# Kernel tuning notes

Hardware: AMD Instinct MI355X
Metric: run time of the kernel (lower is better)

The kernel has to match this reference:

```python
import jax, jax.numpy as jnp
import numpy as np
from jax import lax

B, N, S, K = 16, 8192, 1024, 32
FACTOR = 1.0
EPS_BN = 1e-5


def farthest_point_sample(xyz, npoint):
    # xyz: [B, N, 3] -> idx [B, npoint]. Deterministic start at index 0
    # (torch version starts at a random index; start choice doesn't change the math pattern).
    b, n, _ = xyz.shape
    bidx = jnp.arange(b)

    def step(carry, _):
        distance, farthest = carry
        centroid = xyz[bidx, farthest]                      # [B, 3]
        dist = jnp.sum((xyz - centroid[:, None, :]) ** 2, -1)  # [B, N]
        distance = jnp.minimum(distance, dist)
        new_far = jnp.argmax(distance, axis=-1)
        return (distance, new_far), farthest

    init = (jnp.full((b, n), 1e10, xyz.dtype), jnp.zeros((b,), jnp.int32))
    _, idxs = lax.scan(step, init, None, length=npoint)
    return idxs.T  # [B, npoint]


def square_distance(src, dst):
    # [B,Ns,3] x [B,Nd,3] -> [B,Ns,Nd]
    d = -2.0 * jnp.einsum('bnc,bmc->bnm', src, dst)
    d += jnp.sum(src ** 2, -1)[:, :, None]
    d += jnp.sum(dst ** 2, -1)[:, None, :]
    return d


def safe_cdist(x):
    # x: [B, C, S]; pairwise euclidean over rows -> [B, C, C]; zero-safe sqrt
    diff = x[:, :, None, :] - x[:, None, :, :]          # [B, C, C, S]
    sq = jnp.sum(diff * diff, -1)
    pos = sq > 0
    return jnp.where(pos, jnp.sqrt(jnp.where(pos, sq, 1.0)), 0.0)


def batchnorm(x, gamma, beta, axes):
    mean = jnp.mean(x, axes, keepdims=True)
    var = jnp.var(x, axes, keepdims=True)  # biased, as in torch BN normalization
    return (x - mean) / jnp.sqrt(var + EPS_BN) * gamma + beta


def reference(xyz, bn1_gamma, bn1_beta, bn2_gamma, bn2_beta):
    b = xyz.shape[0]
    # --- FPS sampling ---
    fps_idx = farthest_point_sample(lax.stop_gradient(xyz), S)          # [B,S]
    new_xyz = jnp.take_along_axis(xyz, fps_idx[:, :, None], axis=1)     # [B,S,3]
    # --- kNN grouping ---
    sq = square_distance(lax.stop_gradient(new_xyz), lax.stop_gradient(xyz))  # [B,S,N]
    _, knn_idx = lax.top_k(-sq, K)                                      # [B,S,K] indices
    grouped = jax.vmap(lambda p, i: p[i])(xyz, knn_idx)                 # [B,S,K,3]
    diff = grouped - new_xyz[:, :, None, :]
    std = jnp.std(diff, ddof=1)                                         # scalar, unbiased like torch.std
    knn_norm = diff / (std + 1e-5)
    center = jnp.broadcast_to(new_xyz[:, :, None, :], (b, S, K, 3))
    knn_xyz = jnp.concatenate([knn_norm, center], axis=-1)              # [B,S,K,6]
    # --- Pooling over neighbors ---
    x = jnp.transpose(knn_xyz, (0, 3, 1, 2))                            # [B,6,S,K]
    lc = jnp.max(x, -1) + jnp.mean(x, -1)                               # [B,6,S]
    lc = jax.nn.relu(batchnorm(lc, bn1_gamma[None, :, None], bn1_beta[None, :, None], (0, 2)))
    # --- Consecutive representation (cdist + superdiagonal factor) ---
    tfcw = safe_cdist(lc)                                               # [B,6,6]
    i = jnp.arange(5)
    tfcw = tfcw.at[:, i, i + 1].multiply(FACTOR)
    # --- Pooling2 ---
    feat = tfcw.reshape(b, -1)                                          # [B,36]
    feat = jax.nn.relu(batchnorm(feat, bn2_gamma[None, :], bn2_beta[None, :], (0,)))
    return feat


def setup_inputs() -> dict:
    key = jax.random.key(0)
    k1, = jax.random.split(key, 1)
    return {
        'xyz': jax.random.normal(k1, (B, N, 3), dtype=jnp.float32),
        'bn1_gamma': jnp.ones((6,), jnp.float32),
        'bn1_beta': jnp.zeros((6,), jnp.float32),
        'bn2_gamma': jnp.ones((36,), jnp.float32),
        'bn2_beta': jnp.zeros((36,), jnp.float32),
    }
```

## Files before the change

kernel.cpp:

```cpp
#include <hip/hip_runtime.h>
#include <hip/hip_bf16.h>

constexpr int BB = 16;
constexpr int NN = 8192;
constexpr int SS = 1024;
constexpr int KK = 32;
constexpr int BUFC = 256;

__device__ __forceinline__ float b2f(__hip_bfloat16 h) { return __bfloat162float(h); }

__device__ __forceinline__ unsigned mkey32(float d) {
    unsigned u = __float_as_uint(d);
    return u ^ (0x80000000u | (unsigned)((int)u >> 31));
}

template <int CTRL, int RMASK>
__device__ __forceinline__ unsigned long long dppmove_u64(unsigned long long v) {
    int lo = (int)(unsigned)v, hi = (int)(unsigned)(v >> 32);
    int nlo = __builtin_amdgcn_update_dpp(lo, lo, CTRL, RMASK, 0xf, false);
    int nhi = __builtin_amdgcn_update_dpp(hi, hi, CTRL, RMASK, 0xf, false);
    return ((unsigned long long)(unsigned)nhi << 32) | (unsigned)nlo;
}

__device__ __forceinline__ unsigned long long u64max(unsigned long long a,
                                                     unsigned long long b) {
    return a > b ? a : b;
}

__device__ __forceinline__ unsigned long long wave_max_dpp(unsigned long long k) {
    k = u64max(k, dppmove_u64<0x121, 0xf>(k));
    k = u64max(k, dppmove_u64<0x122, 0xf>(k));
    k = u64max(k, dppmove_u64<0x124, 0xf>(k));
    k = u64max(k, dppmove_u64<0x128, 0xf>(k));
    k = u64max(k, dppmove_u64<0x142, 0xa>(k));
    k = u64max(k, dppmove_u64<0x143, 0xc>(k));
    return k;
}

__device__ __forceinline__ unsigned long long bitonic64(unsigned long long v, int lane) {
#pragma unroll
    for (int k = 2; k <= 64; k <<= 1) {
#pragma unroll
        for (int j = k >> 1; j > 0; j >>= 1) {
            unsigned long long p = __shfl_xor(v, j);
            bool up = ((lane & k) == 0);
            bool lower = ((lane & j) == 0);
            bool take_min = (up == lower);
            v = take_min ? (p < v ? p : v) : (p > v ? p : v);
        }
    }
    return v;
}

__global__ __launch_bounds__(256) void convert_kernel(
    const void* __restrict__ xyz_raw, const void* __restrict__ g1r,
    const void* __restrict__ b1r, const void* __restrict__ g2r,
    const void* __restrict__ b2r, float* __restrict__ xyzf,
    float* __restrict__ params, void* __restrict__ out_raw) {
    const unsigned short* u = (const unsigned short*)xyz_raw;
    unsigned short s = u[2 * (threadIdx.x & 63)];
    int e = (s >> 7) & 0xFF;
    unsigned long long m = __ballot(e >= 100 && e <= 140);
    bool isbf = __popcll(m) > 48;

    const int NT = BB * NN * 3;
    int tid = blockIdx.x * blockDim.x + threadIdx.x;
    int stride = gridDim.x * blockDim.x;
    if (isbf) {
        const __hip_bfloat16* p = (const __hip_bfloat16*)xyz_raw;
        for (int i = tid; i < NT; i += stride) xyzf[i] = b2f(p[i]);
    } else {
        const float* p = (const float*)xyz_raw;
        for (int i = tid; i < NT; i += stride) xyzf[i] = p[i];
    }
    if (blockIdx.x == 0 && threadIdx.x < 85) {
        int t = threadIdx.x;
        if (t == 84) {
            params[84] = isbf ? 1.0f : 0.0f;
        } else {
            const void* src; int off;
            if (t < 6)       { src = g1r; off = t; }
            else if (t < 12) { src = b1r; off = t - 6; }
            else if (t < 48) { src = g2r; off = t - 12; }
            else             { src = b2r; off = t - 48; }
            params[t] = isbf ? b2f(((const __hip_bfloat16*)src)[off])
                             : ((const float*)src)[off];
        }
    }
    if (blockIdx.x == 1 && threadIdx.x < 64) {
        for (int i = threadIdx.x; i < 576; i += 64) {
            if (isbf) ((__hip_bfloat16*)out_raw)[i] = __float2bfloat16(1.0f);
            else      ((float*)out_raw)[i] = 1.0f;
        }
    }
}

__global__ __launch_bounds__(512, 2) void fps_kernel(const float* __restrict__ xyzf,
                                                     float* __restrict__ new_xyz) {
    constexpr int T = 512, P = NN / T;
    const int b = blockIdx.x, t = threadIdx.x;
    const float* xb = xyzf + (size_t)b * NN * 3;

    float px[P], py[P], pz[P], ds[P];
#pragma unroll
    for (int j = 0; j < P; j++) {
        int p = t + j * T;
        px[j] = xb[p * 3 + 0];
        py[j] = xb[p * 3 + 1];
        pz[j] = xb[p * 3 + 2];
        ds[j] = 1e10f;
    }

    __shared__ unsigned long long skey[2][8];

    float cx = xb[0], cy = xb[1], cz = xb[2];
    if (t == 0) {
        float* o = new_xyz + (size_t)b * SS * 3;
        o[0] = cx; o[1] = cy; o[2] = cz;
    }
    const int wave = t >> 6, lane = t & 63;

    for (int step = 1; step < SS; step++) {
        float bv = -1.0f; int bj = 0;
#pragma unroll
        for (int j = 0; j < P; j++) {
            float dx = __fsub_rn(px[j], cx);
            float dy = __fsub_rn(py[j], cy);
            float dz = __fsub_rn(pz[j], cz);
            float d = __fadd_rn(__fadd_rn(__fmul_rn(dx, dx), __fmul_rn(dy, dy)), __fmul_rn(dz, dz));
            float mm = fminf(ds[j], d);
            ds[j] = mm;
            if (mm > bv) { bv = mm; bj = j; }
        }
        unsigned idx = (unsigned)(t + bj * T);
        unsigned long long key =
            ((unsigned long long)__float_as_uint(bv) << 32) | (unsigned)(~idx);

        key = wave_max_dpp(key);
        const int par = step & 1;
        if (lane == 63) skey[par][wave] = key;
        __syncthreads();

        unsigned long long k0 = u64max(skey[par][0], skey[par][1]);
        unsigned long long k1 = u64max(skey[par][2], skey[par][3]);
        unsigned long long k2 = u64max(skey[par][4], skey[par][5]);
        unsigned long long k3 = u64max(skey[par][6], skey[par][7]);
        unsigned long long bk = u64max(u64max(k0, k1), u64max(k2, k3));

        unsigned gidx = ~(unsigned)bk;
        const float* cp = xb + (size_t)gidx * 3;
        cx = cp[0]; cy = cp[1]; cz = cp[2];
        if (t == 0) {
            float* o = new_xyz + ((size_t)b * SS + step) * 3;
            o[0] = cx; o[1] = cy; o[2] = cz;
        }
    }
}

__global__ __launch_bounds__(256, 2) void knn_kernel(const float* __restrict__ xyzf,
                                                     const float* __restrict__ new_xyz,
                                                     float* __restrict__ A,
                                                     double* __restrict__ qstats) {
    __shared__ unsigned long long buf[4][BUFC];
    const int t = threadIdx.x;
    const int lane = t & 63, wv = t >> 6;
    const int w = blockIdx.x * 4 + wv;
    const int b = w >> 10, s = w & 1023;

    const float* q = new_xyz + ((size_t)b * SS + s) * 3;
    float qx = q[0], qy = q[1], qz = q[2];
    float qq = __fadd_rn(__fadd_rn(__fmul_rn(qx, qx), __fmul_rn(qy, qy)), __fmul_rn(qz, qz));

    const float* pb = xyzf + (size_t)b * NN * 3;

    unsigned mk[128];
    unsigned long long lmin = ~0ull;
#pragma unroll
    for (int j = 0; j < 128; j++) {
        int idx = j * 64 + lane;
        float px = pb[idx * 3 + 0];
        float py = pb[idx * 3 + 1];
        float pz = pb[idx * 3 + 2];
        float dot = __fadd_rn(__fadd_rn(__fmul_rn(qx, px), __fmul_rn(qy, py)), __fmul_rn(qz, pz));
        float pp  = __fadd_rn(__fadd_rn(__fmul_rn(px, px), __fmul_rn(py, py)), __fmul_rn(pz, pz));
        float d = __fadd_rn(__fadd_rn(__fmul_rn(-2.0f, dot), qq), pp);
        mk[j] = mkey32(d);
        unsigned long long key = ((unsigned long long)mk[j] << 32) | (unsigned)idx;
        lmin = key < lmin ? key : lmin;
    }

    unsigned long long vs = bitonic64(lmin, lane);
    unsigned long long That = __shfl(vs, 31);

    for (int i = lane; i < BUFC; i += 64) buf[wv][i] = ~0ull;
    const unsigned long long ltmask = (1ull << lane) - 1ull;
    int base = 0;
#pragma unroll
    for (int j = 0; j < 128; j++) {
        unsigned long long key = ((unsigned long long)mk[j] << 32) | (unsigned)(j * 64 + lane);
        bool f = key <= That;
        unsigned long long bal = __ballot(f);
        int pos = base + __popcll(bal & ltmask);
        if (f && pos < BUFC) buf[wv][pos] = key;
        base += __popcll(bal);
    }

    if (base > BUFC) {
        unsigned lo = 0, hi = (unsigned)(That >> 32);
        for (int it = 0; it < 32; it++) {
            unsigned mid = lo + ((hi - lo) >> 1);
            int c = 0;
#pragma unroll
            for (int j = 0; j < 128; j++) c += (mk[j] <= mid) ? 1 : 0;
#pragma unroll
            for (int o = 32; o > 0; o >>= 1) c += __shfl_xor(c, o);
            if (c >= 32) hi = mid; else lo = mid + 1;
        }
        That = ((unsigned long long)hi << 32) | 0xFFFFFFFFull;
        for (int i = lane; i < BUFC; i += 64) buf[wv][i] = ~0ull;
        base = 0;
#pragma unroll
        for (int j = 0; j < 128; j++) {
            unsigned long long key = ((unsigned long long)mk[j] << 32) | (unsigned)(j * 64 + lane);
            bool f = key <= That;
            unsigned long long bal = __ballot(f);
            int pos = base + __popcll(bal & ltmask);
            if (f && pos < BUFC) buf[wv][pos] = key;
            base += __popcll(bal);
        }
        if (base > BUFC) base = BUFC;
    }

    int M = base;
    unsigned long long kept = ~0ull;
    if (M <= 64) {
        unsigned long long v = (lane < M) ? buf[wv][lane] : ~0ull;
        v = bitonic64(v, lane);
        kept = v;
    } else {
        unsigned long long c0 = buf[wv][lane];
        unsigned long long c1 = buf[wv][64 + lane];
        unsigned long long c2 = buf[wv][128 + lane];
        unsigned long long c3 = buf[wv][192 + lane];
        for (int r = 0; r < KK; r++) {
            unsigned long long m01 = c0 < c1 ? c0 : c1;
            unsigned long long m23 = c2 < c3 ? c2 : c3;
            unsigned long long mm = m01 < m23 ? m01 : m23;
#pragma unroll
            for (int o = 32; o > 0; o >>= 1) {
                unsigned long long t2 = __shfl_xor(mm, o);
                mm = t2 < mm ? t2 : mm;
            }
            if (lane == r) kept = mm;
            c0 = (c0 == mm) ? ~0ull : c0;
            c1 = (c1 == mm) ? ~0ull : c1;
            c2 = (c2 == mm) ? ~0ull : c2;
            c3 = (c3 == mm) ? ~0ull : c3;
        }
    }

    bool act = (lane < KK);
    float gx = 0.0f, gy = 0.0f, gz = 0.0f;
    if (act) {
        unsigned nidx = (unsigned)kept;
        gx = pb[nidx * 3 + 0];
        gy = pb[nidx * 3 + 1];
        gz = pb[nidx * 3 + 2];
    }
    float dx = __fsub_rn(gx, qx);
    float dy = __fsub_rn(gy, qy);
    float dz = __fsub_rn(gz, qz);
    float mx = act ? dx : -3.402823466e38f;
    float my = act ? dy : -3.402823466e38f;
    float mz = act ? dz : -3.402823466e38f;
    float sx = act ? dx : 0.0f;
    float sy = act ? dy : 0.0f;
    float sz = act ? dz : 0.0f;
    double s1 = act ? ((double)dx + (double)dy + (double)dz) : 0.0;
    double s2 = act ? ((double)dx * dx + (double)dy * dy + (double)dz * dz) : 0.0;
#pragma unroll
    for (int o = 32; o > 0; o >>= 1) {
        mx = fmaxf(mx, __shfl_xor(mx, o));
        my = fmaxf(my, __shfl_xor(my, o));
        mz = fmaxf(mz, __shfl_xor(mz, o));
        sx += __shfl_xor(sx, o);
        sy += __shfl_xor(sy, o);
        sz += __shfl_xor(sz, o);
        s1 += __shfl_xor(s1, o);
        s2 += __shfl_xor(s2, o);
    }
    if (lane == 0) {
        float* a = A + ((size_t)b * SS + s) * 3;
        a[0] = __fadd_rn(mx, __fmul_rn(sx, 0.03125f));
        a[1] = __fadd_rn(my, __fmul_rn(sy, 0.03125f));
        a[2] = __fadd_rn(mz, __fmul_rn(sz, 0.03125f));
        qstats[2 * w + 0] = s1;
        qstats[2 * w + 1] = s2;
    }
}

__global__ __launch_bounds__(256) void reduce_stats_kernel(const double* __restrict__ qstats,
                                                           double* __restrict__ stats) {
    __shared__ double r1[4], r2[4];
    int t = threadIdx.x;
    double a = 0.0, bsum = 0.0;
    for (int i = t; i < BB * SS; i += 256) { a += qstats[2 * i]; bsum += qstats[2 * i + 1]; }
#pragma unroll
    for (int o = 32; o > 0; o >>= 1) { a += __shfl_xor(a, o); bsum += __shfl_xor(bsum, o); }
    int wv = t >> 6, ln = t & 63;
    if (ln == 0) { r1[wv] = a; r2[wv] = bsum; }
    __syncthreads();
    if (t == 0) {
        stats[0] = r1[0] + r1[1] + r1[2] + r1[3];
        stats[1] = r2[0] + r2[1] + r2[2] + r2[3];
    }
}

__global__ __launch_bounds__(256) void lc_kernel(const float* __restrict__ new_xyz,
                                                 const float* __restrict__ A,
                                                 const double* __restrict__ stats,
                                                 float* __restrict__ lc,
                                                 double* __restrict__ bn1acc) {
    __shared__ double red[4];
    const int b = blockIdx.x / 6, c = blockIdx.x % 6;
    const int t = threadIdx.x;
    const double n = (double)BB * SS * KK * 3;
    double sd = stats[0], sq = stats[1];
    double var = (sq - sd * sd / n) / (n - 1.0);
    float stdv = (float)sqrt(var);
    float denom = __fadd_rn(stdv, 1e-5f);

    double s1 = 0.0, s2 = 0.0;
    for (int r = 0; r < 4; r++) {
        int s = r * 256 + t;
        float v;
        if (c < 3) {
            v = A[((size_t)b * SS + s) * 3 + c] / denom;
        } else {
            float ww = new_xyz[((size_t)b * SS + s) * 3 + (c - 3)];
            v = __fadd_rn(ww, ww);
        }
        lc[((size_t)b * 6 + c) * SS + s] = v;
        s1 += (double)v;
        s2 += (double)v * (double)v;
    }
#pragma unroll
    for (int off = 32; off > 0; off >>= 1) { s1 += __shfl_down(s1, off); s2 += __shfl_down(s2, off); }
    int wv = t >> 6, ln = t & 63;
    if (ln == 0) red[wv] = s1;
    __syncthreads();
    if (t == 0) atomicAdd(&bn1acc[c * 2 + 0], red[0] + red[1] + red[2] + red[3]);
    __syncthreads();
    if (ln == 0) red[wv] = s2;
    __syncthreads();
    if (t == 0) atomicAdd(&bn1acc[c * 2 + 1], red[0] + red[1] + red[2] + red[3]);
}

__global__ __launch_bounds__(256) void cdist_kernel(const float* __restrict__ lc,
                                                    const double* __restrict__ bn1acc,
                                                    const float* __restrict__ params,
                                                    float* __restrict__ tf) {
    __shared__ float sy[6 * SS];
    const int b = blockIdx.x, t = threadIdx.x;
    float mean[6], sde[6], gg[6], bt[6];
    const double n = (double)BB * SS;
#pragma unroll
    for (int c = 0; c < 6; c++) {
        double m = bn1acc[c * 2 + 0] / n;
        double v = bn1acc[c * 2 + 1] / n - m * m;
        mean[c] = (float)m;
        sde[c] = sqrtf((float)v + 1e-5f);
        gg[c] = params[c];
        bt[c] = params[6 + c];
    }
    for (int r = 0; r < 24; r++) {
        int g = r * 256 + t;
        int c = g >> 10;
        float v = lc[(size_t)b * 6 * SS + g];
        float y = (v - mean[c]) / sde[c] * gg[c] + bt[c];
        sy[g] = fmaxf(y, 0.0f);
    }
    __syncthreads();
    if (t < 6) tf[b * 36 + t * 7] = 0.0f;

    const int w = t >> 6, lane = t & 63;
    const int PI[15] = {0,0,0,0,0,1,1,1,1,2,2,2,3,3,4};
    const int PJ[15] = {1,2,3,4,5,2,3,4,5,3,4,5,4,5,5};
    for (int r = 0; r < 4; r++) {
        int p = w + r * 4;
        if (p < 15) {
            int i = PI[p], j = PJ[p];
            float acc = 0.0f;
            for (int m2 = 0; m2 < 16; m2++) {
                int s = lane + m2 * 64;
                float d = sy[i * SS + s] - sy[j * SS + s];
                acc += d * d;
            }
#pragma unroll
            for (int off = 32; off > 0; off >>= 1) acc += __shfl_down(acc, off);
            if (lane == 0) {
                float v = acc > 0.0f ? sqrtf(acc) : 0.0f;
                const float FACTOR = 1.0f;
                tf[b * 36 + i * 6 + j] = (j == i + 1) ? v * FACTOR : v;
                tf[b * 36 + j * 6 + i] = v;
            }
        }
    }
}

__global__ __launch_bounds__(64) void bn2_kernel(const float* __restrict__ tf,
                                                 const float* __restrict__ params,
                                                 void* __restrict__ out_raw) {
    int f = threadIdx.x;
    if (f >= 36) return;
    bool isbf = params[84] != 0.0f;
    float x[16]; float sum = 0.0f;
#pragma unroll
    for (int b = 0; b < 16; b++) { x[b] = tf[b * 36 + f]; sum += x[b]; }
    float mean = sum * 0.0625f;
    float vs = 0.0f;
#pragma unroll
    for (int b = 0; b < 16; b++) { float d = x[b] - mean; vs += d * d; }
    float var = vs * 0.0625f;
    float denom = sqrtf(var + 1e-5f);
    float g = params[12 + f], bb = params[48 + f];
#pragma unroll
    for (int b = 0; b < 16; b++) {
        float y = (x[b] - mean) / denom * g + bb;
        y = fmaxf(y, 0.0f);
        if (isbf) ((__hip_bfloat16*)out_raw)[b * 36 + f] = __float2bfloat16(y);
        else      ((float*)out_raw)[b * 36 + f] = y;
    }
}

extern "C" void kernel_launch(void* const* d_in, const int* in_sizes, int n_in,
                              void* d_out, int out_size, void* d_ws, size_t ws_size,
                              hipStream_t stream) {
    const void* xyz_raw = d_in[0];
    const void* g1r = d_in[1]; const void* b1r = d_in[2];
    const void* g2r = d_in[3]; const void* b2r = d_in[4];
    {
        const void* six[2] = {nullptr, nullptr}; int n6 = 0;
        const void* t36[2] = {nullptr, nullptr}; int n36 = 0;
        const void* big = nullptr;
        for (int i = 0; i < n_in; i++) {
            if (in_sizes[i] == BB * NN * 3) big = d_in[i];
            else if (in_sizes[i] == 6  && n6  < 2) six[n6++]  = d_in[i];
            else if (in_sizes[i] == 36 && n36 < 2) t36[n36++] = d_in[i];
        }
        if (big && n6 == 2 && n36 == 2) {
            xyz_raw = big; g1r = six[0]; b1r = six[1]; g2r = t36[0]; b2r = t36[1];
        }
    }

    char* ws = (char*)d_ws;
    float* xyzf    = (float*)(ws + 0);
    float* new_xyz = (float*)(ws + 1572864);
    float* A       = (float*)(ws + 1769472);
    float* lc      = (float*)(ws + 1966080);
    float* tf      = (float*)(ws + 2359296);
    double* stats  = (double*)(ws + 2361600);
    double* bn1acc = stats + 2;
    float* params  = (float*)(ws + 2361712);
    double* qstats = (double*)(ws + 2362112);

    hipMemsetAsync(stats, 0, 14 * sizeof(double), stream);
    hipLaunchKernelGGL(convert_kernel, dim3(512), dim3(256), 0, stream,
                       xyz_raw, g1r, b1r, g2r, b2r, xyzf, params, d_out);
    hipLaunchKernelGGL(fps_kernel,          dim3(16),   dim3(512), 0, stream, xyzf, new_xyz);
    hipLaunchKernelGGL(knn_kernel,          dim3(4096), dim3(256), 0, stream, xyzf, new_xyz, A, qstats);
    hipLaunchKernelGGL(reduce_stats_kernel, dim3(1),    dim3(256), 0, stream, qstats, stats);
    hipLaunchKernelGGL(lc_kernel,           dim3(96),   dim3(256), 0, stream, new_xyz, A, stats, lc, bn1acc);
    hipLaunchKernelGGL(cdist_kernel,        dim3(16),   dim3(256), 0, stream, lc, bn1acc, params, tf);
    hipLaunchKernelGGL(bn2_kernel,          dim3(1),    dim3(64),  0, stream, tf, params, d_out);

    (void)in_sizes; (void)n_in; (void)out_size; (void)ws_size;
}
```

Measured before the change: 1.336 ms.

## Split FPS per batch across four cooperating blocks with global-memory handshake

Farthest point sampling now spreads each batch over four 256-thread blocks, each owning a quarter of the points, instead of one 512-thread block. Every step, each block publishes its local max (distance, index and step tag packed into 64 bits) to a global slot, then spins on the other three slots to pick the global winner. The goal is to raise parallelism from 16 blocks to 64 and cut per-thread work on the serial FPS critical path. In exchange each step now pays a cross-block global-memory round trip, and the spin wait assumes all four blocks are resident at once, with a guard counter as the only fallback.

```diff
diff --git a/kernel.cpp b/kernel.cpp
--- a/kernel.cpp
+++ b/kernel.cpp
@@ -6,6 +6,7 @@
 constexpr int SS = 1024;
 constexpr int KK = 32;
 constexpr int BUFC = 256;
+constexpr int FC = 4;
 
 __device__ __forceinline__ float b2f(__hip_bfloat16 h) { return __bfloat162float(h); }
 
@@ -56,7 +57,8 @@
     const void* __restrict__ xyz_raw, const void* __restrict__ g1r,
     const void* __restrict__ b1r, const void* __restrict__ g2r,
     const void* __restrict__ b2r, float* __restrict__ xyzf,
-    float* __restrict__ params, void* __restrict__ out_raw) {
+    float* __restrict__ params, void* __restrict__ out_raw,
+    unsigned long long* __restrict__ cand) {
     const unsigned short* u = (const unsigned short*)xyz_raw;
     unsigned short s = u[2 * (threadIdx.x & 63)];
     int e = (s >> 7) & 0xFF;
@@ -93,32 +95,44 @@
             else      ((float*)out_raw)[i] = 1.0f;
         }
     }
-}
-
-__global__ __launch_bounds__(512, 2) void fps_kernel(const float* __restrict__ xyzf,
-                                                     float* __restrict__ new_xyz) {
-    constexpr int T = 512, P = NN / T;
-    const int b = blockIdx.x, t = threadIdx.x;
-    const float* xb = xyzf + (size_t)b * NN * 3;
+    if (blockIdx.x == 2 && threadIdx.x < BB * FC * 2) {
+        cand[threadIdx.x] = 0ull;
+    }
+}
+
+__global__ __launch_bounds__(256) void fps_kernel(const float* __restrict__ xyzf,
+                                                  float* __restrict__ new_xyz,
+                                                  unsigned long long* __restrict__ cand) {
+    constexpr int T = 256, SLICE = NN / FC, P = SLICE / T;
+    const int blk = blockIdx.x;
+    const int batch = blk >> 2, sub = blk & 3;
+    const int t = threadIdx.x;
+    const int base = sub * SLICE;
+    const float* xb = xyzf + (size_t)batch * NN * 3;
 
     float px[P], py[P], pz[P], ds[P];
 #pragma unroll
     for (int j = 0; j < P; j++) {
-        int p = t + j * T;
+        int p = base + t + j * T;
         px[j] = xb[p * 3 + 0];
         py[j] = xb[p * 3 + 1];
         pz[j] = xb[p * 3 + 2];
         ds[j] = 1e10f;
     }
 
-    __shared__ unsigned long long skey[2][8];
+    __shared__ unsigned long long skey[2][4];
 
     float cx = xb[0], cy = xb[1], cz = xb[2];
-    if (t == 0) {
-        float* o = new_xyz + (size_t)b * SS * 3;
+    if (sub == 0 && t == 0) {
+        float* o = new_xyz + (size_t)batch * SS * 3;
         o[0] = cx; o[1] = cy; o[2] = cz;
     }
     const int wave = t >> 6, lane = t & 63;
+
+    unsigned long long* myslot = cand + ((size_t)batch * FC + sub) * 2;
+    unsigned long long* s1p = cand + ((size_t)batch * FC + (sub ^ 1)) * 2;
+    unsigned long long* s2p = cand + ((size_t)batch * FC + (sub ^ 2)) * 2;
+    unsigned long long* s3p = cand + ((size_t)batch * FC + (sub ^ 3)) * 2;
 
     for (int step = 1; step < SS; step++) {
         float bv = -1.0f; int bj = 0;
@@ -132,7 +146,7 @@
             ds[j] = mm;
             if (mm > bv) { bv = mm; bj = j; }
         }
-        unsigned idx = (unsigned)(t + bj * T);
+        unsigned idx = (unsigned)(base + t + bj * T);
         unsigned long long key =
             ((unsigned long long)__float_as_uint(bv) << 32) | (unsigned)(~idx);
 
@@ -141,17 +155,35 @@
         if (lane == 63) skey[par][wave] = key;
         __syncthreads();
 
-        unsigned long long k0 = u64max(skey[par][0], skey[par][1]);
-        unsigned long long k1 = u64max(skey[par][2], skey[par][3]);
-        unsigned long long k2 = u64max(skey[par][4], skey[par][5]);
-        unsigned long long k3 = u64max(skey[par][6], skey[par][7]);
-        unsigned long long bk = u64max(u64max(k0, k1), u64max(k2, k3));
-
-        unsigned gidx = ~(unsigned)bk;
-        const float* cp = xb + (size_t)gidx * 3;
+        unsigned long long bk = u64max(u64max(skey[par][0], skey[par][1]),
+                                       u64max(skey[par][2], skey[par][3]));
+
+        unsigned idxf = ~(unsigned)bk;
+        unsigned long long packed = (bk & 0xFFFFFFFF00000000ull)
+            | ((unsigned long long)((~idxf) & 0x1FFFu) << 19)
+            | (unsigned long long)(unsigned)step;
+
+        if (t == 0)
+            __hip_atomic_store(&myslot[par], packed, __ATOMIC_RELAXED,
+                               __HIP_MEMORY_SCOPE_AGENT);
+
+        unsigned long long v1, v2, v3;
+        int guard = 0;
+        do {
+            v1 = __hip_atomic_load(&s1p[par], __ATOMIC_RELAXED, __HIP_MEMORY_SCOPE_AGENT);
+            v2 = __hip_atomic_load(&s2p[par], __ATOMIC_RELAXED, __HIP_MEMORY_SCOPE_AGENT);
+            v3 = __hip_atomic_load(&s3p[par], __ATOMIC_RELAXED, __HIP_MEMORY_SCOPE_AGENT);
+        } while ((((unsigned)(v1 & 0x7FFFFu) != (unsigned)step) ||
+                  ((unsigned)(v2 & 0x7FFFFu) != (unsigned)step) ||
+                  ((unsigned)(v3 & 0x7FFFFu) != (unsigned)step)) &&
+                 ++guard < (1 << 20));
+
+        unsigned long long best = u64max(u64max(packed, v1), u64max(v2, v3));
+        unsigned widx = 8191u - (unsigned)((best >> 19) & 0x1FFFu);
+        const float* cp = xb + (size_t)widx * 3;
         cx = cp[0]; cy = cp[1]; cz = cp[2];
-        if (t == 0) {
-            float* o = new_xyz + ((size_t)b * SS + step) * 3;
+        if (sub == 0 && t == 0) {
+            float* o = new_xyz + ((size_t)batch * SS + step) * 3;
             o[0] = cx; o[1] = cy; o[2] = cz;
         }
     }
@@ -463,16 +495,17 @@
     double* bn1acc = stats + 2;
     float* params  = (float*)(ws + 2361712);
     double* qstats = (double*)(ws + 2362112);
+    unsigned long long* cand = (unsigned long long*)(ws + 1966080);
 
     hipMemsetAsync(stats, 0, 14 * sizeof(double), stream);
     hipLaunchKernelGGL(convert_kernel, dim3(512), dim3(256), 0, stream,
-                       xyz_raw, g1r, b1r, g2r, b2r, xyzf, params, d_out);
-    hipLaunchKernelGGL(fps_kernel,          dim3(16),   dim3(512), 0, stream, xyzf, new_xyz);
-    hipLaunchKernelGGL(knn_kernel,          dim3(4096), dim3(256), 0, stream, xyzf, new_xyz, A, qstats);
-    hipLaunchKernelGGL(reduce_stats_kernel, dim3(1),    dim3(256), 0, stream, qstats, stats);
-    hipLaunchKernelGGL(lc_kernel,           dim3(96),   dim3(256), 0, stream, new_xyz, A, stats, lc, bn1acc);
-    hipLaunchKernelGGL(cdist_kernel,        dim3(16),   dim3(256), 0, stream, lc, bn1acc, params, tf);
-    hipLaunchKernelGGL(bn2_kernel,          dim3(1),    dim3(64),  0, stream, tf, params, d_out);
+                       xyz_raw, g1r, b1r, g2r, b2r, xyzf, params, d_out, cand);
+    hipLaunchKernelGGL(fps_kernel,          dim3(BB * FC), dim3(256), 0, stream, xyzf, new_xyz, cand);
+    hipLaunchKernelGGL(knn_kernel,          dim3(4096),    dim3(256), 0, stream, xyzf, new_xyz, A, qstats);
+    hipLaunchKernelGGL(reduce_stats_kernel, dim3(1),       dim3(256), 0, stream, qstats, stats);
+    hipLaunchKernelGGL(lc_kernel,           dim3(96),      dim3(256), 0, stream, new_xyz, A, stats, lc, bn1acc);
+    hipLaunchKernelGGL(cdist_kernel,        dim3(16),      dim3(256), 0, stream, lc, bn1acc, params, tf);
+    hipLaunchKernelGGL(bn2_kernel,          dim3(1),       dim3(64),  0, stream, tf, params, d_out);
 
     (void)in_sizes; (void)n_in; (void)out_size; (void)ws_size;
 }
```

New measurement: 1.940 ms. 45.2% more time.
